# Performance work log

Measured on AMD Instinct MI355X. Metric: run time of the kernel, lower is better.

## Reference

```python
import jax, jax.numpy as jnp
import numpy as np
import math

KEY_SIZE = 128  # init arg; scale = 1/sqrt(key_size)


def setup_inputs() -> dict:
    key = jax.random.key(0)
    kq, kk, kv = jax.random.split(key, 3)
    B, LQ, LK, D, DV = 16, 2048, 2048, 128, 128
    q = jax.random.normal(kq, (B, LQ, D), dtype=jnp.float32)
    k = jax.random.normal(kk, (B, LK, D), dtype=jnp.float32)
    v = jax.random.normal(kv, (B, LK, DV), dtype=jnp.float32)
    return {"q": q, "k": k, "v": v}


def reference(q, k, v):
    scale = 1.0 / math.sqrt(KEY_SIZE)
    # scores: [B, Lq, Lk]
    scores = jnp.einsum('bqd,bkd->bqk', q, k) * scale
    probs = jax.nn.softmax(scores, axis=-1)
    # dropout with p=0.0 is identity (eval-equivalent)
    return jnp.einsum('bqk,bkv->bqv', probs, v)
```

## Files before the change

### kernel.cpp

```cpp
#include <hip/hip_runtime.h>
#include <hip/hip_bf16.h>

typedef float f32x4 __attribute__((ext_vector_type(4)));
typedef float f32x16 __attribute__((ext_vector_type(16)));
typedef short bf16x8 __attribute__((ext_vector_type(8)));
typedef unsigned u32x4 __attribute__((ext_vector_type(4)));

constexpr int NB = 16, LQ = 2048, LK = 2048, D = 128, DV = 128;
constexpr int KVBLK = 32;
constexpr int NTH = 32;
constexpr float SCALE = 0.08838834764831843f;
constexpr float LOG2E = 1.4426950408889634f;
constexpr float QSCALE = SCALE * LOG2E;

__device__ __forceinline__ unsigned short f2bfs(float f) {
  __hip_bfloat16 h = __float2bfloat16(f);
  return __builtin_bit_cast(unsigned short, h);
}

__device__ __forceinline__ unsigned short f2bf(float f) {
  unsigned int u = __float_as_uint(f);
  u += 0x7FFFu + ((u >> 16) & 1u);
  return (unsigned short)(u >> 16);
}

__device__ __forceinline__ int swz2(int row) {
  return (row ^ (row >> 1) ^ (row >> 3)) & 7;
}

__device__ __forceinline__ int swap23(int m) {
  return (m & ~12) | ((m & 4) << 1) | ((m & 8) >> 1);
}

typedef const __attribute__((address_space(1))) void* gas1_t;
typedef __attribute__((address_space(3))) void* las3_t;
__device__ __forceinline__ void gload16(const void* g, void* l) {
  __builtin_amdgcn_global_load_lds((gas1_t)g, (las3_t)l, 16, 0, 0);
}

__device__ __forceinline__ unsigned pk2(float lo, float hi) {
  unsigned short a = f2bfs(lo), b = f2bfs(hi);
  return (unsigned)a | ((unsigned)b << 16);
}

__device__ __forceinline__ void mk_pb(const f32x16& s, bf16x8& pe, bf16x8& po) {
  u32x4 e = {pk2(s[0], s[1]), pk2(s[2], s[3]), pk2(s[4], s[5]), pk2(s[6], s[7])};
  pe = __builtin_bit_cast(bf16x8, e);
  u32x4 od = {pk2(s[8], s[9]), pk2(s[10], s[11]), pk2(s[12], s[13]), pk2(s[14], s[15])};
  po = __builtin_bit_cast(bf16x8, od);
}

__global__ __launch_bounds__(256) void conv_bf16(const float* __restrict__ in,
                                                 unsigned short* __restrict__ out,
                                                 float scale) {
  int i = blockIdx.x * 256 + threadIdx.x;
  f32x4 a = ((const f32x4*)in)[2 * i];
  f32x4 b = ((const f32x4*)in)[2 * i + 1];
  bf16x8 r;
  #pragma unroll
  for (int j = 0; j < 4; ++j) {
    r[j]     = (short)f2bfs(a[j] * scale);
    r[4 + j] = (short)f2bfs(b[j] * scale);
  }
  ((bf16x8*)out)[i] = r;
}

__global__ __launch_bounds__(256) void conv_vt(const float* __restrict__ v,
                                               unsigned short* __restrict__ vt) {
  __shared__ __align__(16) unsigned short tb[64 * 64];
  const int tid = threadIdx.x;
  const int k0 = blockIdx.x * 64, dv0 = blockIdx.y * 64, b = blockIdx.z;
  {
    const int kk = tid >> 2, dd0 = (tid & 3) * 16;
    const float* src = v + ((long)(b * LK + k0 + kk)) * DV + dv0 + dd0;
    f32x4 a0 = ((const f32x4*)src)[0];
    f32x4 a1 = ((const f32x4*)src)[1];
    f32x4 a2 = ((const f32x4*)src)[2];
    f32x4 a3 = ((const f32x4*)src)[3];
    bf16x8 r0, r1;
    #pragma unroll
    for (int j = 0; j < 4; ++j) {
      r0[j] = (short)f2bfs(a0[j]); r0[4 + j] = (short)f2bfs(a1[j]);
      r1[j] = (short)f2bfs(a2[j]); r1[4 + j] = (short)f2bfs(a3[j]);
    }
    int ch = dd0 >> 3;
    *(bf16x8*)&tb[kk * 64 + ((ch ^ swz2(kk)) << 3)] = r0;
    *(bf16x8*)&tb[kk * 64 + (((ch + 1) ^ swz2(kk)) << 3)] = r1;
  }
  __syncthreads();
  {
    const int dv = tid >> 2, ks = (tid & 3) * 16;
    bf16x8 w0, w1;
    #pragma unroll
    for (int j = 0; j < 8; ++j) {
      int r0 = ks + j, r1 = ks + 8 + j;
      w0[j] = (short)tb[r0 * 64 + (((dv >> 3) ^ swz2(r0)) << 3) + (dv & 7)];
      w1[j] = (short)tb[r1 * 64 + (((dv >> 3) ^ swz2(r1)) << 3) + (dv & 7)];
    }
    unsigned short* dst = vt + ((long)(b * DV + dv0 + dv)) * LK + k0 + ks;
    *(bf16x8*)dst = w0;
    *(bf16x8*)(dst + 8) = w1;
  }
}

__global__ __launch_bounds__(256, 2) void attn_fwd6(
    const float* __restrict__ qp, const unsigned short* __restrict__ wsK,
    const unsigned short* __restrict__ wsVt, float* __restrict__ op) {
  __shared__ __align__(16) unsigned short sm[32768];

  const int tid = threadIdx.x;
  const int wid = tid >> 6;
  const int h2  = wid >> 1;
  const int lane = tid & 63;
  const int q32 = lane & 31;
  const int hi  = lane >> 5;
  const int ht  = tid & 127;

  const int bid = blockIdx.x;
  const int sbid = (bid & 7) * 64 + (bid >> 3);
  const int b = sbid >> 5;
  const int qb = (sbid & 31) * 64;
  const int qwave = qb + (wid & 1) * 32;

  bf16x8 aq[8];
  {
    const float* qrow = qp + ((long)(b * LQ + qwave + q32)) * D + hi * 8;
    #pragma unroll
    for (int st = 0; st < 8; ++st) {
      f32x4 x0 = *(const f32x4*)(qrow + st * 16);
      f32x4 x1 = *(const f32x4*)(qrow + st * 16 + 4);
      #pragma unroll
      for (int j = 0; j < 4; ++j) {
        aq[st][j]     = (short)f2bfs(x0[j] * QSCALE);
        aq[st][4 + j] = (short)f2bfs(x1[j] * QSCALE);
      }
    }
  }
  __builtin_amdgcn_sched_barrier(0);

  const unsigned short* kbatch = wsK + (long)b * LK * D;
  const unsigned short* vbatch = wsVt + (long)b * DV * LK;
  const int kvbase = h2 * 1024;
  const int lbase = h2 * 16384;

  const unsigned short* ksp[4];
  const unsigned short* vsp[4];
  unsigned ldk[4], ldv[4];
  #pragma unroll
  for (int it = 0; it < 4; ++it) {
    int ci = it * 128 + ht;
    int krow = ci >> 4, kc16 = ci & 15;
    ksp[it] = kbatch + ((long)kvbase + swap23(krow)) * D +
              ((kc16 ^ swz2(krow)) << 3);
    ldk[it] = lbase + ci * 8;
    int r64 = ci >> 3, ch = ci & 7;
    int L = ch ^ swz2(r64);
    int dv = 2 * r64 + (L >> 2), kc = L & 3;
    vsp[it] = vbatch + (long)dv * LK + kvbase + kc * 8;
    ldv[it] = lbase + 4096 + ci * 8;
  }

  auto stage = [&](int buf, int t) {
    const int lb = buf * 8192;
    #pragma unroll
    for (int it = 0; it < 4; ++it)
      gload16(ksp[it] + t * (KVBLK * D), &sm[ldk[it] + lb]);
    #pragma unroll
    for (int it = 0; it < 4; ++it)
      gload16(vsp[it] + t * KVBLK, &sm[ldv[it] + lb]);
  };

  stage(0, 0);
  stage(1, 1);

  f32x16 o[4];
  #pragma unroll
  for (int mt = 0; mt < 4; ++mt) o[mt] = (f32x16){};
  float m_s = -1e30f, l_s = 0.f;

  for (int t = 0; t < NTH; ++t) {
    if (t < NTH - 1) {
      asm volatile("s_waitcnt vmcnt(8)" ::: "memory");
    } else {
      asm volatile("s_waitcnt vmcnt(0)" ::: "memory");
    }
    __builtin_amdgcn_sched_barrier(0);
    __builtin_amdgcn_s_barrier();
    __builtin_amdgcn_sched_barrier(0);

    const int cur = t & 1;
    const int kb = lbase + cur * 8192, vb = kb + 4096;

    f32x16 s0 = (f32x16){};
    __builtin_amdgcn_s_setprio(1);
    #pragma unroll
    for (int st = 0; st < 8; ++st) {
      const int c16 = 2 * st + hi;
      bf16x8 k0 = *(const bf16x8*)&sm[kb + q32 * 128 + ((c16 ^ swz2(q32)) << 3)];
      s0 = __builtin_amdgcn_mfma_f32_32x32x16_bf16(k0, aq[st], s0, 0, 0, 0);
    }
    __builtin_amdgcn_s_setprio(0);

    bf16x8 vf[8];
    #pragma unroll
    for (int ks = 0; ks < 2; ++ks) {
      #pragma unroll
      for (int mt = 0; mt < 4; ++mt) {
        const int row = mt * 32 + q32;
        const int r64 = row >> 1;
        const int L = (row & 1) * 4 + 2 * ks + hi;
        vf[ks * 4 + mt] = *(const bf16x8*)&sm[vb + r64 * 64 + ((L ^ swz2(r64)) << 3)];
      }
    }

    float m8[8];
    #pragma unroll
    for (int i = 0; i < 8; ++i) m8[i] = fmaxf(s0[i], s0[i + 8]);
    float m4a = fmaxf(m8[0], m8[1]), m4b = fmaxf(m8[2], m8[3]);
    float m4c = fmaxf(m8[4], m8[5]), m4d = fmaxf(m8[6], m8[7]);
    float pm = fmaxf(fmaxf(m4a, m4b), fmaxf(m4c, m4d));
    pm = fmaxf(pm, __shfl_xor(pm, 32));
    if (!__all(pm <= m_s + 8.0f)) {
      float mn = fmaxf(m_s, pm);
      float al = exp2f(m_s - mn);
      l_s *= al;
      #pragma unroll
      for (int mt = 0; mt < 4; ++mt)
        #pragma unroll
        for (int i = 0; i < 16; ++i) o[mt][i] *= al;
      m_s = mn;
    }
    #pragma unroll
    for (int i = 0; i < 16; ++i) s0[i] = exp2f(s0[i] - m_s);
    float s8[8];
    #pragma unroll
    for (int i = 0; i < 8; ++i) s8[i] = s0[i] + s0[i + 8];
    float s4a = (s8[0] + s8[1]) + (s8[2] + s8[3]);
    float s4b = (s8[4] + s8[5]) + (s8[6] + s8[7]);
    float sum = s4a + s4b;
    l_s += sum + __shfl_xor(sum, 32);

    bf16x8 pb0, pb1;
    mk_pb(s0, pb0, pb1);

    __builtin_amdgcn_s_setprio(1);
    #pragma unroll
    for (int mt = 0; mt < 4; ++mt)
      o[mt] = __builtin_amdgcn_mfma_f32_32x32x16_bf16(vf[mt], pb0, o[mt], 0, 0, 0);
    #pragma unroll
    for (int mt = 0; mt < 4; ++mt)
      o[mt] = __builtin_amdgcn_mfma_f32_32x32x16_bf16(vf[4 + mt], pb1, o[mt], 0, 0, 0);
    __builtin_amdgcn_s_setprio(0);

    __builtin_amdgcn_sched_barrier(0);
    __builtin_amdgcn_s_barrier();
    __builtin_amdgcn_sched_barrier(0);

    if (t < NTH - 2) stage(cur, t + 2);
  }

  float* scr = (float*)sm;
  float* wreg = scr + (size_t)(wid & 1) * 4352;
  __syncthreads();
  if (h2 == 1) {
    #pragma unroll
    for (int j4 = 0; j4 < 16; ++j4) {
      const int mt = j4 >> 2, a = j4 & 3;
      f32x4 v = {o[mt][4 * a], o[mt][4 * a + 1], o[mt][4 * a + 2], o[mt][4 * a + 3]};
      *(f32x4*)&wreg[lane * 64 + ((j4 ^ (lane & 15)) << 2)] = v;
    }
    wreg[4096 + lane * 2] = m_s;
    wreg[4096 + lane * 2 + 1] = l_s;
  }
  __syncthreads();
  if (h2 == 0) {
    const float m1 = wreg[4096 + lane * 2];
    const float l1 = wreg[4096 + lane * 2 + 1];
    const float mm = fmaxf(m_s, m1);
    float a0 = exp2f(m_s - mm), a1 = exp2f(m1 - mm);
    const float inv = 1.f / (a0 * l_s + a1 * l1);
    a0 *= inv;
    a1 *= inv;
    float* dst = op + ((long)(b * LQ + qwave + q32)) * DV;
    #pragma unroll
    for (int j4 = 0; j4 < 16; ++j4) {
      const int mt = j4 >> 2, a = j4 & 3;
      f32x4 pv = *(const f32x4*)&wreg[lane * 64 + ((j4 ^ (lane & 15)) << 2)];
      f32x4 r;
      #pragma unroll
      for (int i = 0; i < 4; ++i) r[i] = a0 * o[mt][4 * a + i] + a1 * pv[i];
      *(f32x4*)&dst[32 * mt + 8 * a + 4 * hi] = r;
    }
  }
}

__device__ __forceinline__ int swzc(int row, int c16) {
  return c16 ^ ((row ^ (row >> 3)) & 7);
}

__global__ __launch_bounds__(256, 2) void attn_fwd(
    const float* __restrict__ qp, const float* __restrict__ kp,
    const float* __restrict__ vp, float* __restrict__ op) {
  __shared__ __align__(16) unsigned short smm[28672];
  const int tid = threadIdx.x, wid = tid >> 6, lane = tid & 63;
  const int g = lane >> 4, c = lane & 15;
  const int b = blockIdx.y, qb = blockIdx.x * 64;
  const float* qg = qp + ((long)b * LQ + qb) * D;
  const float* kg = kp + (long)b * LK * D;
  const float* vg = vp + (long)b * LK * DV;
  #pragma unroll
  for (int it = 0; it < 4; ++it) {
    int ch = it * 256 + tid, row = ch >> 4, c16 = ch & 15;
    const float* src = qg + row * D + c16 * 8;
    f32x4 f0 = *(const f32x4*)(src);
    f32x4 f1 = *(const f32x4*)(src + 4);
    bf16x8 fr;
    #pragma unroll
    for (int j = 0; j < 4; ++j) {
      fr[j] = (short)f2bf(f0[j] * SCALE);
      fr[4 + j] = (short)f2bf(f1[j] * SCALE);
    }
    *(bf16x8*)&smm[row * 128 + swzc(row, c16) * 8] = fr;
  }
  __syncthreads();
  bf16x8 aq[4];
  #pragma unroll
  for (int ks = 0; ks < 4; ++ks) {
    int row = wid * 16 + c;
    aq[ks] = *(const bf16x8*)&smm[row * 128 + swzc(row, ks * 4 + g) * 8];
  }
  f32x4 o[8]; f32x4 fz = {0.f, 0.f, 0.f, 0.f};
  #pragma unroll
  for (int i = 0; i < 8; ++i) o[i] = fz;
  float m_r[4] = {-1e30f, -1e30f, -1e30f, -1e30f};
  float l_r[4] = {0.f, 0.f, 0.f, 0.f};
  const int pbase = 24576 + wid * 1024;
  for (int kv0 = 0; kv0 < LK; kv0 += 64) {
    __syncthreads();
    const float* ksrc = kg + (long)kv0 * D;
    #pragma unroll
    for (int it = 0; it < 4; ++it) {
      int ch = it * 256 + tid, row = ch >> 4, c16 = ch & 15;
      const float* src = ksrc + row * D + c16 * 8;
      f32x4 f0 = *(const f32x4*)(src);
      f32x4 f1 = *(const f32x4*)(src + 4);
      bf16x8 fr;
      #pragma unroll
      for (int j = 0; j < 4; ++j) { fr[j] = (short)f2bf(f0[j]); fr[4 + j] = (short)f2bf(f1[j]); }
      *(bf16x8*)&smm[8192 + row * 128 + swzc(row, c16) * 8] = fr;
    }
    {
      const float* vsrc = vg + (long)kv0 * DV;
      int dvq = (tid & 31) * 4, kg8 = tid >> 5;
      f32x4 col[8];
      #pragma unroll
      for (int j = 0; j < 8; ++j) col[j] = *(const f32x4*)(vsrc + (kg8 * 8 + j) * DV + dvq);
      #pragma unroll
      for (int i = 0; i < 4; ++i) {
        int dv = dvq + i;
        bf16x8 fr;
        #pragma unroll
        for (int j = 0; j < 8; ++j) fr[j] = (short)f2bf(col[j][i]);
        *(bf16x8*)&smm[16384 + dv * 64 + swzc(dv, kg8) * 8] = fr;
      }
    }
    __syncthreads();
    f32x4 s[4];
    #pragma unroll
    for (int i = 0; i < 4; ++i) s[i] = fz;
    #pragma unroll
    for (int ks = 0; ks < 4; ++ks) {
      #pragma unroll
      for (int t = 0; t < 4; ++t) {
        int row = t * 16 + c;
        bf16x8 bk = *(const bf16x8*)&smm[8192 + row * 128 + swzc(row, ks * 4 + g) * 8];
        s[t] = __builtin_amdgcn_mfma_f32_16x16x32_bf16(aq[ks], bk, s[t], 0, 0, 0);
      }
    }
    #pragma unroll
    for (int r = 0; r < 4; ++r) {
      float pm = fmaxf(fmaxf(s[0][r], s[1][r]), fmaxf(s[2][r], s[3][r]));
      pm = fmaxf(pm, __shfl_xor(pm, 1));
      pm = fmaxf(pm, __shfl_xor(pm, 2));
      pm = fmaxf(pm, __shfl_xor(pm, 4));
      pm = fmaxf(pm, __shfl_xor(pm, 8));
      float mn = fmaxf(m_r[r], pm);
      float al = exp2f((m_r[r] - mn) * LOG2E);
      float sum = 0.f;
      #pragma unroll
      for (int t = 0; t < 4; ++t) {
        float p = exp2f((s[t][r] - mn) * LOG2E);
        s[t][r] = p; sum += p;
      }
      sum += __shfl_xor(sum, 1); sum += __shfl_xor(sum, 2);
      sum += __shfl_xor(sum, 4); sum += __shfl_xor(sum, 8);
      l_r[r] = l_r[r] * al + sum; m_r[r] = mn;
      #pragma unroll
      for (int dvt = 0; dvt < 8; ++dvt) o[dvt][r] *= al;
    }
    #pragma unroll
    for (int t = 0; t < 4; ++t)
      #pragma unroll
      for (int r = 0; r < 4; ++r) {
        int row = g * 4 + r, colx = c + 16 * t;
        smm[pbase + row * 64 + swzc(row, colx >> 3) * 8 + (colx & 7)] = f2bf(s[t][r]);
      }
    #pragma unroll
    for (int ks = 0; ks < 2; ++ks) {
      bf16x8 pa = *(const bf16x8*)&smm[pbase + c * 64 + swzc(c, ks * 4 + g) * 8];
      #pragma unroll
      for (int dvt = 0; dvt < 8; ++dvt) {
        int row = dvt * 16 + c;
        bf16x8 vb2 = *(const bf16x8*)&smm[16384 + row * 64 + swzc(row, ks * 4 + g) * 8];
        o[dvt] = __builtin_amdgcn_mfma_f32_16x16x32_bf16(pa, vb2, o[dvt], 0, 0, 0);
      }
    }
  }
  float* dst = op + ((long)b * LQ + qb + wid * 16) * DV;
  #pragma unroll
  for (int r = 0; r < 4; ++r) {
    float inv = 1.f / l_r[r];
    #pragma unroll
    for (int dvt = 0; dvt < 8; ++dvt)
      dst[(g * 4 + r) * DV + dvt * 16 + c] = o[dvt][r] * inv;
  }
}

extern "C" void kernel_launch(void* const* d_in, const int* in_sizes, int n_in,
                              void* d_out, int out_size, void* d_ws, size_t ws_size,
                              hipStream_t stream) {
  const float* q = (const float*)d_in[0];
  const float* k = (const float*)d_in[1];
  const float* v = (const float*)d_in[2];
  float* out = (float*)d_out;

  const size_t kelems = (size_t)NB * LK * D;
  const size_t need = kelems * 2 * 2;
  if (ws_size >= need) {
    unsigned short* wsK = (unsigned short*)d_ws;
    unsigned short* wsVt = wsK + kelems;
    conv_bf16<<<dim3((int)(kelems / 8 / 256)), dim3(256), 0, stream>>>(k, wsK, 1.0f);
    conv_vt<<<dim3(LK / 64, DV / 64, NB), dim3(256), 0, stream>>>(v, wsVt);
    attn_fwd6<<<dim3(NB * LQ / 64), dim3(256), 0, stream>>>(q, wsK, wsVt, out);
  } else {
    attn_fwd<<<dim3(LQ / 64, NB), dim3(256), 0, stream>>>(q, k, v, out);
  }
}
```

Baseline: 79.43 us.

## Pre-pack K and V into MFMA fragment order so tiles stream contiguously

The K and V conversion kernels now write bf16 data already arranged per 32-row tile in the exact order the attention kernel's MFMA fragment loads consume. Each tile is then staged with contiguous 16-byte global-to-LDS copies, and the LDS reads use simple linear offsets with no XOR swizzle or address arithmetic. This removes per-iteration index math and strided global reads of the transposed V. The risk is LDS bank conflicts, since the swizzle is gone, and a slower V conversion kernel, which now does scalar 2-byte LDS stores.

Result: faster. 76.80 us (-3.3%).

```diff
diff --git a/kernel.cpp b/kernel.cpp
--- a/kernel.cpp
+++ b/kernel.cpp
@@ -7,7 +7,6 @@
 typedef unsigned u32x4 __attribute__((ext_vector_type(4)));
 
 constexpr int NB = 16, LQ = 2048, LK = 2048, D = 128, DV = 128;
-constexpr int KVBLK = 32;
 constexpr int NTH = 32;
 constexpr float SCALE = 0.08838834764831843f;
 constexpr float LOG2E = 1.4426950408889634f;
@@ -50,62 +49,64 @@
   po = __builtin_bit_cast(bf16x8, od);
 }
 
-__global__ __launch_bounds__(256) void conv_bf16(const float* __restrict__ in,
-                                                 unsigned short* __restrict__ out,
-                                                 float scale) {
-  int i = blockIdx.x * 256 + threadIdx.x;
-  f32x4 a = ((const f32x4*)in)[2 * i];
-  f32x4 b = ((const f32x4*)in)[2 * i + 1];
-  bf16x8 r;
+__global__ __launch_bounds__(256) void conv_k2(const float* __restrict__ kp,
+                                               unsigned short* __restrict__ out) {
+  __shared__ __align__(16) unsigned short tk[4096];
+  const int T = blockIdx.x, b = blockIdx.y;
+  const int tid = threadIdx.x;
+  const int k = tid >> 3, cc = tid & 7, d0 = cc * 16;
+  const float* src = kp + ((long)(b * LK) + 32 * T + k) * D + d0;
+  f32x4 a0 = ((const f32x4*)src)[0];
+  f32x4 a1 = ((const f32x4*)src)[1];
+  f32x4 a2 = ((const f32x4*)src)[2];
+  f32x4 a3 = ((const f32x4*)src)[3];
+  bf16x8 r0, r1;
   #pragma unroll
   for (int j = 0; j < 4; ++j) {
-    r[j]     = (short)f2bfs(a[j] * scale);
-    r[4 + j] = (short)f2bfs(b[j] * scale);
-  }
-  ((bf16x8*)out)[i] = r;
-}
-
-__global__ __launch_bounds__(256) void conv_vt(const float* __restrict__ v,
-                                               unsigned short* __restrict__ vt) {
-  __shared__ __align__(16) unsigned short tb[64 * 64];
+    r0[j] = (short)f2bfs(a0[j]); r0[4 + j] = (short)f2bfs(a1[j]);
+    r1[j] = (short)f2bfs(a2[j]); r1[4 + j] = (short)f2bfs(a3[j]);
+  }
+  const int rr = swap23(k);
+  *(bf16x8*)&tk[(2 * cc) * 256 + rr * 8] = r0;
+  *(bf16x8*)&tk[(2 * cc + 1) * 256 + rr * 8] = r1;
+  __syncthreads();
+  unsigned short* dst = out + ((long)(b * 64 + T)) * 4096 + tid * 16;
+  *(bf16x8*)dst = *(const bf16x8*)&tk[tid * 16];
+  *(bf16x8*)(dst + 8) = *(const bf16x8*)&tk[tid * 16 + 8];
+}
+
+__global__ __launch_bounds__(256) void conv_v2(const float* __restrict__ vp,
+                                               unsigned short* __restrict__ out) {
+  __shared__ __align__(16) unsigned short tv[4096];
+  const int T = blockIdx.x, b = blockIdx.y;
   const int tid = threadIdx.x;
-  const int k0 = blockIdx.x * 64, dv0 = blockIdx.y * 64, b = blockIdx.z;
-  {
-    const int kk = tid >> 2, dd0 = (tid & 3) * 16;
-    const float* src = v + ((long)(b * LK + k0 + kk)) * DV + dv0 + dd0;
-    f32x4 a0 = ((const f32x4*)src)[0];
-    f32x4 a1 = ((const f32x4*)src)[1];
-    f32x4 a2 = ((const f32x4*)src)[2];
-    f32x4 a3 = ((const f32x4*)src)[3];
-    bf16x8 r0, r1;
-    #pragma unroll
-    for (int j = 0; j < 4; ++j) {
-      r0[j] = (short)f2bfs(a0[j]); r0[4 + j] = (short)f2bfs(a1[j]);
-      r1[j] = (short)f2bfs(a2[j]); r1[4 + j] = (short)f2bfs(a3[j]);
-    }
-    int ch = dd0 >> 3;
-    *(bf16x8*)&tb[kk * 64 + ((ch ^ swz2(kk)) << 3)] = r0;
-    *(bf16x8*)&tb[kk * 64 + (((ch + 1) ^ swz2(kk)) << 3)] = r1;
-  }
+  const int k = tid >> 3, cc = tid & 7, d0 = cc * 16;
+  const float* src = vp + ((long)(b * LK) + 32 * T + k) * DV + d0;
+  f32x4 a0 = ((const f32x4*)src)[0];
+  f32x4 a1 = ((const f32x4*)src)[1];
+  f32x4 a2 = ((const f32x4*)src)[2];
+  f32x4 a3 = ((const f32x4*)src)[3];
+  unsigned short vals[16];
+  #pragma unroll
+  for (int j = 0; j < 4; ++j) {
+    vals[j]      = f2bfs(a0[j]);
+    vals[4 + j]  = f2bfs(a1[j]);
+    vals[8 + j]  = f2bfs(a2[j]);
+    vals[12 + j] = f2bfs(a3[j]);
+  }
+  const int vbase = (k >> 3) * 1024 + (k & 7);
+  #pragma unroll
+  for (int i = 0; i < 16; ++i)
+    tv[vbase + (d0 + i) * 8] = vals[i];
   __syncthreads();
-  {
-    const int dv = tid >> 2, ks = (tid & 3) * 16;
-    bf16x8 w0, w1;
-    #pragma unroll
-    for (int j = 0; j < 8; ++j) {
-      int r0 = ks + j, r1 = ks + 8 + j;
-      w0[j] = (short)tb[r0 * 64 + (((dv >> 3) ^ swz2(r0)) << 3) + (dv & 7)];
-      w1[j] = (short)tb[r1 * 64 + (((dv >> 3) ^ swz2(r1)) << 3) + (dv & 7)];
-    }
-    unsigned short* dst = vt + ((long)(b * DV + dv0 + dv)) * LK + k0 + ks;
-    *(bf16x8*)dst = w0;
-    *(bf16x8*)(dst + 8) = w1;
-  }
-}
-
-__global__ __launch_bounds__(256, 2) void attn_fwd6(
-    const float* __restrict__ qp, const unsigned short* __restrict__ wsK,
-    const unsigned short* __restrict__ wsVt, float* __restrict__ op) {
+  unsigned short* dst = out + ((long)(b * 64 + T)) * 4096 + tid * 16;
+  *(bf16x8*)dst = *(const bf16x8*)&tv[tid * 16];
+  *(bf16x8*)(dst + 8) = *(const bf16x8*)&tv[tid * 16 + 8];
+}
+
+__global__ __launch_bounds__(256, 2) void attn_fwd7(
+    const float* __restrict__ qp, const unsigned short* __restrict__ wsK2,
+    const unsigned short* __restrict__ wsV2, float* __restrict__ op) {
   __shared__ __align__(16) unsigned short sm[32768];
 
   const int tid = threadIdx.x;
@@ -138,36 +139,23 @@
   }
   __builtin_amdgcn_sched_barrier(0);
 
-  const unsigned short* kbatch = wsK + (long)b * LK * D;
-  const unsigned short* vbatch = wsVt + (long)b * DV * LK;
-  const int kvbase = h2 * 1024;
   const int lbase = h2 * 16384;
-
-  const unsigned short* ksp[4];
-  const unsigned short* vsp[4];
-  unsigned ldk[4], ldv[4];
-  #pragma unroll
-  for (int it = 0; it < 4; ++it) {
-    int ci = it * 128 + ht;
-    int krow = ci >> 4, kc16 = ci & 15;
-    ksp[it] = kbatch + ((long)kvbase + swap23(krow)) * D +
-              ((kc16 ^ swz2(krow)) << 3);
-    ldk[it] = lbase + ci * 8;
-    int r64 = ci >> 3, ch = ci & 7;
-    int L = ch ^ swz2(r64);
-    int dv = 2 * r64 + (L >> 2), kc = L & 3;
-    vsp[it] = vbatch + (long)dv * LK + kvbase + kc * 8;
-    ldv[it] = lbase + 4096 + ci * 8;
-  }
+  const unsigned short* kps = wsK2 + ((long)(b * 64 + h2 * 32)) * 4096;
+  const unsigned short* vps = wsV2 + ((long)(b * 64 + h2 * 32)) * 4096;
 
   auto stage = [&](int buf, int t) {
-    const int lb = buf * 8192;
-    #pragma unroll
-    for (int it = 0; it < 4; ++it)
-      gload16(ksp[it] + t * (KVBLK * D), &sm[ldk[it] + lb]);
-    #pragma unroll
-    for (int it = 0; it < 4; ++it)
-      gload16(vsp[it] + t * KVBLK, &sm[ldv[it] + lb]);
+    const long toff = (long)t * 4096;
+    const int lb = lbase + buf * 8192;
+    #pragma unroll
+    for (int it = 0; it < 4; ++it) {
+      const int ci = it * 128 + ht;
+      gload16(kps + toff + ci * 8, &sm[lb + ci * 8]);
+    }
+    #pragma unroll
+    for (int it = 0; it < 4; ++it) {
+      const int ci = it * 128 + ht;
+      gload16(vps + toff + ci * 8, &sm[lb + 4096 + ci * 8]);
+    }
   };
 
   stage(0, 0);
@@ -177,6 +165,9 @@
   #pragma unroll
   for (int mt = 0; mt < 4; ++mt) o[mt] = (f32x16){};
   float m_s = -1e30f, l_s = 0.f;
+
+  const int kub = lbase + hi * 256 + q32 * 8;
+  const int vub = lbase + 4096 + hi * 1024 + q32 * 8;
 
   for (int t = 0; t < NTH; ++t) {
     if (t < NTH - 1) {
@@ -189,29 +180,24 @@
     __builtin_amdgcn_sched_barrier(0);
 
     const int cur = t & 1;
-    const int kb = lbase + cur * 8192, vb = kb + 4096;
+    const int kb = kub + cur * 8192;
+    const int vb = vub + cur * 8192;
 
     f32x16 s0 = (f32x16){};
     __builtin_amdgcn_s_setprio(1);
     #pragma unroll
     for (int st = 0; st < 8; ++st) {
-      const int c16 = 2 * st + hi;
-      bf16x8 k0 = *(const bf16x8*)&sm[kb + q32 * 128 + ((c16 ^ swz2(q32)) << 3)];
+      bf16x8 k0 = *(const bf16x8*)&sm[kb + st * 512];
       s0 = __builtin_amdgcn_mfma_f32_32x32x16_bf16(k0, aq[st], s0, 0, 0, 0);
     }
     __builtin_amdgcn_s_setprio(0);
 
     bf16x8 vf[8];
     #pragma unroll
-    for (int ks = 0; ks < 2; ++ks) {
-      #pragma unroll
-      for (int mt = 0; mt < 4; ++mt) {
-        const int row = mt * 32 + q32;
-        const int r64 = row >> 1;
-        const int L = (row & 1) * 4 + 2 * ks + hi;
-        vf[ks * 4 + mt] = *(const bf16x8*)&sm[vb + r64 * 64 + ((L ^ swz2(r64)) << 3)];
-      }
-    }
+    for (int ks = 0; ks < 2; ++ks)
+      #pragma unroll
+      for (int mt = 0; mt < 4; ++mt)
+        vf[ks * 4 + mt] = *(const bf16x8*)&sm[vb + ks * 2048 + mt * 256];
 
     float m8[8];
     #pragma unroll
@@ -437,11 +423,11 @@
   const size_t kelems = (size_t)NB * LK * D;
   const size_t need = kelems * 2 * 2;
   if (ws_size >= need) {
-    unsigned short* wsK = (unsigned short*)d_ws;
-    unsigned short* wsVt = wsK + kelems;
-    conv_bf16<<<dim3((int)(kelems / 8 / 256)), dim3(256), 0, stream>>>(k, wsK, 1.0f);
-    conv_vt<<<dim3(LK / 64, DV / 64, NB), dim3(256), 0, stream>>>(v, wsVt);
-    attn_fwd6<<<dim3(NB * LQ / 64), dim3(256), 0, stream>>>(q, wsK, wsVt, out);
+    unsigned short* wsK2 = (unsigned short*)d_ws;
+    unsigned short* wsV2 = wsK2 + kelems;
+    conv_k2<<<dim3(LK / 32, NB), dim3(256), 0, stream>>>(k, wsK2);
+    conv_v2<<<dim3(LK / 32, NB), dim3(256), 0, stream>>>(v, wsV2);
+    attn_fwd7<<<dim3(NB * LQ / 64), dim3(256), 0, stream>>>(q, wsK2, wsV2, out);
   } else {
     attn_fwd<<<dim3(LQ / 64, NB), dim3(256), 0, stream>>>(q, k, v, out);
   }
```
